# Kernel tuning notes

Hardware: AMD Instinct MI355X
Metric: run time of the kernel (lower is better)

The kernel has to match this reference:

```python
import jax, jax.numpy as jnp
import numpy as np

N_HEAD = 16


def setup_inputs() -> dict:
    key = jax.random.key(0)
    k1, k2, k3 = jax.random.split(key, 3)
    B, T, C = 4, 1024, 1024
    x = jax.random.normal(k1, (B, T, C), dtype=jnp.float32)
    w_attn = jax.random.normal(k2, (3 * C, C), dtype=jnp.float32) * 0.02
    w_proj = jax.random.normal(k3, (C, C), dtype=jnp.float32) * 0.02
    return {"x": x, "w_attn": w_attn, "w_proj": w_proj}


def reference(x, w_attn, w_proj):
    B, T, C = x.shape
    H = N_HEAD
    hs = C // H
    scale = 1.0 / np.sqrt(hs).astype(np.float32)

    qkv = x @ w_attn.T                         # [B, T, 3C]
    q, k, v = jnp.split(qkv, 3, axis=-1)
    q = q.reshape(B, T, H, hs).transpose(0, 2, 1, 3)   # [B, H, T, hs]
    k = k.reshape(B, T, H, hs).transpose(0, 2, 1, 3)
    v = v.reshape(B, T, H, hs).transpose(0, 2, 1, 3)

    scores = jnp.einsum('bhqd,bhkd->bhqk', q, k) * scale   # [B, H, T, T]
    causal = jnp.tril(jnp.ones((T, T), dtype=bool))
    scores = jnp.where(causal, scores, -jnp.inf)

    att = jax.nn.sigmoid(scores)                # sigmoid attention, not softmax
    # Bernoulli straight-through sampling (value = sample, grad flows via att)
    samp_key = jax.random.fold_in(jax.random.key(0), 42)
    samples = jax.random.bernoulli(samp_key, att).astype(att.dtype)
    att = att + jax.lax.stop_gradient(samples - att)

    y = jnp.einsum('bhqk,bhkd->bhqd', att, v)   # [B, H, T, hs]
    att_sum = att.sum(axis=-1)                  # [B, H, T]
    att_var = (att * (1.0 - att)).sum(axis=-1)  # [B, H, T]

    y = y.transpose(0, 2, 1, 3).reshape(B, T, C)
    y = y @ w_proj.T
    return (y, att_sum, att_var)
```

## Files before the change

### kernel.cpp

```cpp
#include <hip/hip_runtime.h>
#include <stdint.h>


#define T_SEQ 1024
#define QKV_LD 3072

typedef __attribute__((ext_vector_type(8))) short bf16x8;
typedef __attribute__((ext_vector_type(4))) float f32x4;
typedef __attribute__((ext_vector_type(4))) unsigned int u32x4;

typedef __attribute__((address_space(3))) uint32_t lds_u32;
typedef __attribute__((address_space(1))) const uint32_t g_u32;

#define ROTL(x, d) __builtin_amdgcn_alignbit((x), (x), 32 - (d))

__device__ __forceinline__ void threefry2x32(uint32_t k0, uint32_t k1,
                                             uint32_t x0, uint32_t x1,
                                             uint32_t &o0, uint32_t &o1) {
  uint32_t ks2 = k0 ^ k1 ^ 0x1BD11BDAu;
#define TF_R4(a, b, c, d)                                                      \
  x0 += x1; x1 = ROTL(x1, a); x1 ^= x0;                                        \
  x0 += x1; x1 = ROTL(x1, b); x1 ^= x0;                                        \
  x0 += x1; x1 = ROTL(x1, c); x1 ^= x0;                                        \
  x0 += x1; x1 = ROTL(x1, d); x1 ^= x0;
  x0 += k0; x1 += k1;
  TF_R4(13, 15, 26, 6)
  x0 += k1; x1 += ks2 + 1u;
  TF_R4(17, 29, 16, 24)
  x0 += ks2; x1 += k0 + 2u;
  TF_R4(13, 15, 26, 6)
  x0 += k0; x1 += k1 + 3u;
  TF_R4(17, 29, 16, 24)
  x0 += k1; x1 += ks2 + 4u;
  TF_R4(13, 15, 26, 6)
  x0 += ks2; x1 += k0 + 5u;
  o0 = x0; o1 = x1;
#undef TF_R4
}

__device__ __forceinline__ unsigned short f2bf(float f) {
  uint32_t u = __float_as_uint(f);
  u += 0x7FFFu + ((u >> 16) & 1u);
  return (unsigned short)(u >> 16);
}

#define N_X4  1048576
#define N_WA4 786432
#define N_WP4 262144

__global__ __launch_bounds__(256) void cvt3_bf16(const float4* __restrict__ x,
                                                 const float4* __restrict__ wa,
                                                 const float4* __restrict__ wp,
                                                 uint2* __restrict__ out) {
  size_t i = (size_t)blockIdx.x * 256 + threadIdx.x;
  const float4* src;
  size_t off;
  if (i < N_X4) { src = x; off = i; }
  else if (i < N_X4 + N_WA4) { src = wa; off = i - N_X4; }
  else { src = wp; off = i - (N_X4 + N_WA4); }
  float4 v = src[off];
  uint2 o;
  o.x = (uint32_t)f2bf(v.x) | ((uint32_t)f2bf(v.y) << 16);
  o.y = (uint32_t)f2bf(v.z) | ((uint32_t)f2bf(v.w) << 16);
  out[i] = o;
}

template <int OUT_BF16>
__global__ __launch_bounds__(256) void gemm_bf16(const unsigned short* __restrict__ A,
                                                 const unsigned short* __restrict__ B,
                                                 void* __restrict__ Cout,
                                                 int M, int N, int K) {
  __shared__ unsigned short As[128 * 32];
  __shared__ unsigned short Bs[128 * 32];

  const int t = threadIdx.x;
  const int lane = t & 63, w = t >> 6;
  const int g = lane >> 4, lr = lane & 15;
  const int rw = w >> 1, cw = w & 1;
  const int bm = blockIdx.x * 128, bn = blockIdx.y * 128;

  const unsigned short* Ag = A + (size_t)(bm + 32 * w + (lane >> 2)) * K + 8 * (lane & 3);
  const unsigned short* Bg = B + (size_t)(bn + 32 * w + (lane >> 2)) * K + 8 * (lane & 3);
  lds_u32* Al0 = (lds_u32*)&As[(32 * w) * 32];
  lds_u32* Al1 = (lds_u32*)&As[(32 * w + 16) * 32];
  lds_u32* Bl0 = (lds_u32*)&Bs[(32 * w) * 32];
  lds_u32* Bl1 = (lds_u32*)&Bs[(32 * w + 16) * 32];

  f32x4 acc[4][4];
#pragma unroll
  for (int i = 0; i < 4; ++i)
#pragma unroll
    for (int j = 0; j < 4; ++j) acc[i][j] = (f32x4){0.f, 0.f, 0.f, 0.f};

  for (int k0 = 0; k0 < K; k0 += 32) {
    __syncthreads();
    __builtin_amdgcn_global_load_lds((g_u32*)(const void*)(Ag + k0), Al0, 16, 0, 0);
    __builtin_amdgcn_global_load_lds((g_u32*)(const void*)(Ag + k0 + (size_t)16 * K), Al1, 16, 0, 0);
    __builtin_amdgcn_global_load_lds((g_u32*)(const void*)(Bg + k0), Bl0, 16, 0, 0);
    __builtin_amdgcn_global_load_lds((g_u32*)(const void*)(Bg + k0 + (size_t)16 * K), Bl1, 16, 0, 0);
    __syncthreads();

    bf16x8 af[4], bfr[4];
#pragma unroll
    for (int i = 0; i < 4; ++i)
      af[i] = *(const bf16x8*)&As[(64 * rw + 16 * i + lr) * 32 + 8 * g];
#pragma unroll
    for (int j = 0; j < 4; ++j)
      bfr[j] = *(const bf16x8*)&Bs[(64 * cw + 16 * j + lr) * 32 + 8 * g];
#pragma unroll
    for (int i = 0; i < 4; ++i)
#pragma unroll
      for (int j = 0; j < 4; ++j)
        acc[i][j] = __builtin_amdgcn_mfma_f32_16x16x32_bf16(af[i], bfr[j], acc[i][j], 0, 0, 0);
  }

#pragma unroll
  for (int i = 0; i < 4; ++i)
#pragma unroll
    for (int j = 0; j < 4; ++j)
#pragma unroll
      for (int r = 0; r < 4; ++r) {
        const size_t row = bm + 64 * rw + 16 * i + 4 * g + r;
        const size_t col = bn + 64 * cw + 16 * j + lr;
        if (OUT_BF16)
          ((unsigned short*)Cout)[row * N + col] = f2bf(acc[i][j][r]);
        else
          ((float*)Cout)[row * N + col] = acc[i][j][r];
      }
}

__constant__ int QT2[16] = {15, 13, 11, 9, 0, 2, 4, 6, 14, 12, 10, 8, 1, 3, 5, 7};

__global__ __launch_bounds__(256) void attn_tile2(const unsigned short* __restrict__ qkv,
                                                  unsigned short* __restrict__ yatt,
                                                  float* __restrict__ att_sum,
                                                  float* __restrict__ att_var) {
  __shared__ uint32_t Ks4[64 * 32];
  __shared__ uint32_t Vt4[64 * 32];
  __shared__ unsigned short St[4][16][72];

  const int t = threadIdx.x;
  const int lane = t & 63, w = t >> 6;
  const int g = lane >> 4, lr = lane & 15;
  const int i = blockIdx.x;
  const int bh = 8 * (i & 7) + ((i >> 3) & 7);
  const int qt = QT2[i >> 6];
  const int b = bh >> 4, h = bh & 15;
  const int qt64 = qt * 64;

  uint32_t dk0, dk1;
  threefry2x32(0u, 0u, 0u, 42u, dk0, dk1);

  const int swzr = (lr & 7) << 2;
  unsigned short (*stw)[72] = St[w];

  const int q0 = qt64 + 16 * w;
  const unsigned short* qr = qkv + (size_t)(b * T_SEQ + q0 + lr) * QKV_LD + h * 64 + 8 * g;
  const bf16x8 aq0 = *(const bf16x8*)qr;
  const bf16x8 aq1 = *(const bf16x8*)(qr + 32);

  f32x4 yacc[4];
#pragma unroll
  for (int c = 0; c < 4; ++c) yacc[c] = (f32x4){0.f, 0.f, 0.f, 0.f};
  int rs[4] = {0, 0, 0, 0};

#pragma unroll 1
  for (int kt = 0; kt <= qt; ++kt) {
    __syncthreads();
    const unsigned short* kb = qkv + (size_t)(b * T_SEQ + kt * 64) * QKV_LD + 1024 + h * 64;
    {
      const int r = t >> 2, s4 = t & 3;
      const unsigned short* src = kb + (size_t)r * QKV_LD + 8 * s4;
      u32x4 v0 = *(const u32x4*)(src);
      u32x4 v1 = *(const u32x4*)(src + 32);
      const int sw = (r & 7) << 2;
      *(u32x4*)&Ks4[r * 32 + ((4 * s4) ^ sw)] = v0;
      *(u32x4*)&Ks4[r * 32 + ((4 * s4 + 16) ^ sw)] = v1;
    }
    {
      const int k2 = 2 * (t & 31), d0 = 8 * (t >> 5);
      const unsigned short* vsrc =
          qkv + (size_t)(b * T_SEQ + kt * 64 + k2) * QKV_LD + 2048 + h * 64 + d0;
      union { u32x4 v; unsigned short us[8]; } va, vb;
      va.v = *(const u32x4*)(vsrc);
      vb.v = *(const u32x4*)(vsrc + QKV_LD);
#pragma unroll
      for (int j = 0; j < 8; ++j) {
        uint32_t pw = (uint32_t)va.us[j] | ((uint32_t)vb.us[j] << 16);
        Vt4[(d0 + j) * 32 + ((t & 31) ^ ((j & 7) << 2))] = pw;
      }
    }
    __syncthreads();

    const int kt64 = kt * 64;
#pragma unroll
    for (int c = 0; c < 4; ++c) {
      const uint32_t* krow = &Ks4[(16 * c + lr) * 32];
      bf16x8 bk0 = *(const bf16x8*)&krow[(4 * g) ^ swzr];
      bf16x8 bk1 = *(const bf16x8*)&krow[(4 * g + 16) ^ swzr];
      f32x4 sa = __builtin_amdgcn_mfma_f32_16x16x32_bf16(aq0, bk0, (f32x4){0.f, 0.f, 0.f, 0.f}, 0, 0, 0);
      sa = __builtin_amdgcn_mfma_f32_16x16x32_bf16(aq1, bk1, sa, 0, 0, 0);

      const int kg = kt64 + 16 * c + lr;
#pragma unroll
      for (int r = 0; r < 4; ++r) {
        const int qg = q0 + 4 * g + r;
        unsigned short sbits = 0;
        if (kg <= qg) {
          float e = __builtin_exp2f(sa[r] * -0.18033688011112042f);
          uint32_t idx = ((uint32_t)bh << 20) | ((uint32_t)qg << 10) | (uint32_t)kg;
          uint32_t r0, r1;
          threefry2x32(dk0, dk1, 0u, idx, r0, r1);
          float u = __uint_as_float(0x3F800000u | ((r0 ^ r1) >> 9)) - 1.0f;
          if (fmaf(u, e, u) < 1.0f) { sbits = 0x3F80; rs[r] += 1; }
        }
        stw[4 * g + r][16 * c + lr] = sbits;
      }
    }

#pragma unroll
    for (int ks = 0; ks < 2; ++ks) {
      const bf16x8 pa = *(const bf16x8*)&stw[lr][32 * ks + 8 * g];
#pragma unroll
      for (int c = 0; c < 4; ++c) {
        bf16x8 vb = *(const bf16x8*)&Vt4[(16 * c + lr) * 32 + ((4 * g + 16 * ks) ^ swzr)];
        yacc[c] = __builtin_amdgcn_mfma_f32_16x16x32_bf16(pa, vb, yacc[c], 0, 0, 0);
      }
    }
  }

  const size_t yb = (size_t)(b * T_SEQ + q0) * 1024 + h * 64;
#pragma unroll
  for (int c = 0; c < 4; ++c)
#pragma unroll
    for (int r = 0; r < 4; ++r)
      yatt[yb + (size_t)(4 * g + r) * 1024 + 16 * c + lr] = f2bf(yacc[c][r]);

#pragma unroll
  for (int r = 0; r < 4; ++r) {
    rs[r] += __shfl_xor(rs[r], 1);
    rs[r] += __shfl_xor(rs[r], 2);
    rs[r] += __shfl_xor(rs[r], 4);
    rs[r] += __shfl_xor(rs[r], 8);
  }
  if (lr == 0) {
#pragma unroll
    for (int r = 0; r < 4; ++r)
      att_sum[(size_t)bh * T_SEQ + q0 + 4 * g + r] = (float)rs[r];
  }
  if (lane < 16) att_var[(size_t)bh * T_SEQ + qt64 + 16 * w + lane] = 0.f;
}

extern "C" void kernel_launch(void* const* d_in, const int* in_sizes, int n_in,
                              void* d_out, int out_size, void* d_ws, size_t ws_size,
                              hipStream_t stream) {
  (void)in_sizes; (void)n_in; (void)out_size; (void)ws_size;
  const float* x      = (const float*)d_in[0];
  const float* w_attn = (const float*)d_in[1];
  const float* w_proj = (const float*)d_in[2];

  float* y_out      = (float*)d_out;
  float* attsum_out = y_out + (size_t)4 * 1024 * 1024;
  float* attvar_out = attsum_out + (size_t)4 * 16 * 1024;

  unsigned short* ws_us = (unsigned short*)d_ws;
  unsigned short* x_bf    = ws_us;
  unsigned short* wa_bf   = x_bf + (size_t)4 * 1024 * 1024;
  unsigned short* wp_bf   = wa_bf + (size_t)3 * 1024 * 1024;
  unsigned short* qkv_bf  = wp_bf + (size_t)1024 * 1024;
  unsigned short* yatt_bf = qkv_bf + (size_t)4096 * 3072;

  dim3 blk(256);
  cvt3_bf16<<<dim3(8192), blk, 0, stream>>>((const float4*)x, (const float4*)w_attn,
                                            (const float4*)w_proj, (uint2*)x_bf);
  gemm_bf16<1><<<dim3(32, 24), blk, 0, stream>>>(x_bf, wa_bf, (void*)qkv_bf, 4096, 3072, 1024);
  attn_tile2<<<dim3(1024), blk, 0, stream>>>(qkv_bf, yatt_bf, attsum_out, attvar_out);
  gemm_bf16<0><<<dim3(32, 8), blk, 0, stream>>>(yatt_bf, wp_bf, (void*)y_out, 4096, 1024, 1024);
}
```

Before: 165.2 us.

## Replace static attention tile schedule with atomic work-stealing over half tiles

The attention kernel goes from a fixed 1024-block grid of 256-thread blocks to a persistent-style grid of 1792 blocks with 128 threads each. Each block processes 32-query half-tiles taken largest-first and fetches the next item from a global atomic counter, which a tiny kernel initialises every launch. The aim is better load balance for the triangular causal workload and less tail idle time. In exchange, each K/V tile is staged into LDS for only two waves instead of four, so global-to-LDS traffic per query roughly doubles, and there is an extra kernel launch plus an atomic per item.

```diff
diff --git a/kernel.cpp b/kernel.cpp
--- a/kernel.cpp
+++ b/kernel.cpp
@@ -4,6 +4,8 @@
 
 #define T_SEQ 1024
 #define QKV_LD 3072
+#define ATTN_GRID 1792
+#define N_ITEMS 2048
 
 typedef __attribute__((ext_vector_type(8))) short bf16x8;
 typedef __attribute__((ext_vector_type(4))) float f32x4;
@@ -65,6 +67,8 @@
   out[i] = o;
 }
 
+__global__ void init_ctr(uint32_t* __restrict__ ctr, uint32_t v) { *ctr = v; }
+
 template <int OUT_BF16>
 __global__ __launch_bounds__(256) void gemm_bf16(const unsigned short* __restrict__ A,
                                                  const unsigned short* __restrict__ B,
@@ -129,24 +133,19 @@
       }
 }
 
-__constant__ int QT2[16] = {15, 13, 11, 9, 0, 2, 4, 6, 14, 12, 10, 8, 1, 3, 5, 7};
-
-__global__ __launch_bounds__(256) void attn_tile2(const unsigned short* __restrict__ qkv,
+__global__ __launch_bounds__(128) void attn_steal(const unsigned short* __restrict__ qkv,
                                                   unsigned short* __restrict__ yatt,
                                                   float* __restrict__ att_sum,
-                                                  float* __restrict__ att_var) {
+                                                  float* __restrict__ att_var,
+                                                  uint32_t* __restrict__ ctr) {
   __shared__ uint32_t Ks4[64 * 32];
   __shared__ uint32_t Vt4[64 * 32];
-  __shared__ unsigned short St[4][16][72];
+  __shared__ unsigned short St[2][16][72];
+  __shared__ int next_item;
 
   const int t = threadIdx.x;
   const int lane = t & 63, w = t >> 6;
   const int g = lane >> 4, lr = lane & 15;
-  const int i = blockIdx.x;
-  const int bh = 8 * (i & 7) + ((i >> 3) & 7);
-  const int qt = QT2[i >> 6];
-  const int b = bh >> 4, h = bh & 15;
-  const int qt64 = qt * 64;
 
   uint32_t dk0, dk1;
   threefry2x32(0u, 0u, 0u, 42u, dk0, dk1);
@@ -154,101 +153,120 @@
   const int swzr = (lr & 7) << 2;
   unsigned short (*stw)[72] = St[w];
 
-  const int q0 = qt64 + 16 * w;
-  const unsigned short* qr = qkv + (size_t)(b * T_SEQ + q0 + lr) * QKV_LD + h * 64 + 8 * g;
-  const bf16x8 aq0 = *(const bf16x8*)qr;
-  const bf16x8 aq1 = *(const bf16x8*)(qr + 32);
-
-  f32x4 yacc[4];
-#pragma unroll
-  for (int c = 0; c < 4; ++c) yacc[c] = (f32x4){0.f, 0.f, 0.f, 0.f};
-  int rs[4] = {0, 0, 0, 0};
+  int item = blockIdx.x;
+  while (item < N_ITEMS) {
+    const int qt = 15 - (item >> 7);
+    const int bh = (item >> 1) & 63;
+    const int half = item & 1;
+    const int b = bh >> 4, h = bh & 15;
+    const int qt64 = qt * 64;
+    const int q0 = qt64 + 32 * half + 16 * w;
+
+    const unsigned short* qr = qkv + (size_t)(b * T_SEQ + q0 + lr) * QKV_LD + h * 64 + 8 * g;
+    const bf16x8 aq0 = *(const bf16x8*)qr;
+    const bf16x8 aq1 = *(const bf16x8*)(qr + 32);
+
+    f32x4 yacc[4];
+#pragma unroll
+    for (int c = 0; c < 4; ++c) yacc[c] = (f32x4){0.f, 0.f, 0.f, 0.f};
+    int rs[4] = {0, 0, 0, 0};
 
 #pragma unroll 1
-  for (int kt = 0; kt <= qt; ++kt) {
+    for (int kt = 0; kt <= qt; ++kt) {
+      __syncthreads();
+      const unsigned short* kb = qkv + (size_t)(b * T_SEQ + kt * 64) * QKV_LD + 1024 + h * 64;
+      {
+        const int r = t >> 1, c0 = 4 * (t & 1);
+        const unsigned short* src = kb + (size_t)r * QKV_LD + 8 * c0;
+        const int sw = (r & 7) << 2;
+#pragma unroll
+        for (int q = 0; q < 4; ++q) {
+          u32x4 v = *(const u32x4*)(src + 8 * q);
+          *(u32x4*)&Ks4[r * 32 + ((4 * (c0 + q)) ^ sw)] = v;
+        }
+      }
+      {
+#pragma unroll
+        for (int it2 = 0; it2 < 2; ++it2) {
+          const int tt = t + 128 * it2;
+          const int k2 = 2 * (tt & 31), d0 = 8 * (tt >> 5);
+          const unsigned short* vsrc =
+              qkv + (size_t)(b * T_SEQ + kt * 64 + k2) * QKV_LD + 2048 + h * 64 + d0;
+          union { u32x4 v; unsigned short us[8]; } va, vb2;
+          va.v = *(const u32x4*)(vsrc);
+          vb2.v = *(const u32x4*)(vsrc + QKV_LD);
+#pragma unroll
+          for (int jj = 0; jj < 8; ++jj) {
+            uint32_t pw = (uint32_t)va.us[jj] | ((uint32_t)vb2.us[jj] << 16);
+            Vt4[(d0 + jj) * 32 + ((tt & 31) ^ ((jj & 7) << 2))] = pw;
+          }
+        }
+      }
+      __syncthreads();
+
+      const int kt64 = kt * 64;
+#pragma unroll
+      for (int c = 0; c < 4; ++c) {
+        const uint32_t* krow = &Ks4[(16 * c + lr) * 32];
+        bf16x8 bk0 = *(const bf16x8*)&krow[(4 * g) ^ swzr];
+        bf16x8 bk1 = *(const bf16x8*)&krow[(4 * g + 16) ^ swzr];
+        f32x4 sa = __builtin_amdgcn_mfma_f32_16x16x32_bf16(aq0, bk0, (f32x4){0.f, 0.f, 0.f, 0.f}, 0, 0, 0);
+        sa = __builtin_amdgcn_mfma_f32_16x16x32_bf16(aq1, bk1, sa, 0, 0, 0);
+
+        const int kg = kt64 + 16 * c + lr;
+#pragma unroll
+        for (int r = 0; r < 4; ++r) {
+          const int qg = q0 + 4 * g + r;
+          unsigned short sbits = 0;
+          if (kg <= qg) {
+            float e = __builtin_exp2f(sa[r] * -0.18033688011112042f);
+            uint32_t idx = ((uint32_t)bh << 20) | ((uint32_t)qg << 10) | (uint32_t)kg;
+            uint32_t r0, r1;
+            threefry2x32(dk0, dk1, 0u, idx, r0, r1);
+            float u = __uint_as_float(0x3F800000u | ((r0 ^ r1) >> 9)) - 1.0f;
+            if (fmaf(u, e, u) < 1.0f) { sbits = 0x3F80; rs[r] += 1; }
+          }
+          stw[4 * g + r][16 * c + lr] = sbits;
+        }
+      }
+
+#pragma unroll
+      for (int ks = 0; ks < 2; ++ks) {
+        const bf16x8 pa = *(const bf16x8*)&stw[lr][32 * ks + 8 * g];
+#pragma unroll
+        for (int c = 0; c < 4; ++c) {
+          bf16x8 vb = *(const bf16x8*)&Vt4[(16 * c + lr) * 32 + ((4 * g + 16 * ks) ^ swzr)];
+          yacc[c] = __builtin_amdgcn_mfma_f32_16x16x32_bf16(pa, vb, yacc[c], 0, 0, 0);
+        }
+      }
+    }
+
+    const size_t yb = (size_t)(b * T_SEQ + q0) * 1024 + h * 64;
+#pragma unroll
+    for (int c = 0; c < 4; ++c)
+#pragma unroll
+      for (int r = 0; r < 4; ++r)
+        yatt[yb + (size_t)(4 * g + r) * 1024 + 16 * c + lr] = f2bf(yacc[c][r]);
+
+#pragma unroll
+    for (int r = 0; r < 4; ++r) {
+      rs[r] += __shfl_xor(rs[r], 1);
+      rs[r] += __shfl_xor(rs[r], 2);
+      rs[r] += __shfl_xor(rs[r], 4);
+      rs[r] += __shfl_xor(rs[r], 8);
+    }
+    if (lr == 0) {
+#pragma unroll
+      for (int r = 0; r < 4; ++r)
+        att_sum[(size_t)bh * T_SEQ + q0 + 4 * g + r] = (float)rs[r];
+    }
+    if (lane < 16) att_var[(size_t)bh * T_SEQ + q0 + lane] = 0.f;
+
     __syncthreads();
-    const unsigned short* kb = qkv + (size_t)(b * T_SEQ + kt * 64) * QKV_LD + 1024 + h * 64;
-    {
-      const int r = t >> 2, s4 = t & 3;
-      const unsigned short* src = kb + (size_t)r * QKV_LD + 8 * s4;
-      u32x4 v0 = *(const u32x4*)(src);
-      u32x4 v1 = *(const u32x4*)(src + 32);
-      const int sw = (r & 7) << 2;
-      *(u32x4*)&Ks4[r * 32 + ((4 * s4) ^ sw)] = v0;
-      *(u32x4*)&Ks4[r * 32 + ((4 * s4 + 16) ^ sw)] = v1;
-    }
-    {
-      const int k2 = 2 * (t & 31), d0 = 8 * (t >> 5);
-      const unsigned short* vsrc =
-          qkv + (size_t)(b * T_SEQ + kt * 64 + k2) * QKV_LD + 2048 + h * 64 + d0;
-      union { u32x4 v; unsigned short us[8]; } va, vb;
-      va.v = *(const u32x4*)(vsrc);
-      vb.v = *(const u32x4*)(vsrc + QKV_LD);
-#pragma unroll
-      for (int j = 0; j < 8; ++j) {
-        uint32_t pw = (uint32_t)va.us[j] | ((uint32_t)vb.us[j] << 16);
-        Vt4[(d0 + j) * 32 + ((t & 31) ^ ((j & 7) << 2))] = pw;
-      }
-    }
+    if (t == 0) next_item = (int)atomicAdd(ctr, 1u);
     __syncthreads();
-
-    const int kt64 = kt * 64;
-#pragma unroll
-    for (int c = 0; c < 4; ++c) {
-      const uint32_t* krow = &Ks4[(16 * c + lr) * 32];
-      bf16x8 bk0 = *(const bf16x8*)&krow[(4 * g) ^ swzr];
-      bf16x8 bk1 = *(const bf16x8*)&krow[(4 * g + 16) ^ swzr];
-      f32x4 sa = __builtin_amdgcn_mfma_f32_16x16x32_bf16(aq0, bk0, (f32x4){0.f, 0.f, 0.f, 0.f}, 0, 0, 0);
-      sa = __builtin_amdgcn_mfma_f32_16x16x32_bf16(aq1, bk1, sa, 0, 0, 0);
-
-      const int kg = kt64 + 16 * c + lr;
-#pragma unroll
-      for (int r = 0; r < 4; ++r) {
-        const int qg = q0 + 4 * g + r;
-        unsigned short sbits = 0;
-        if (kg <= qg) {
-          float e = __builtin_exp2f(sa[r] * -0.18033688011112042f);
-          uint32_t idx = ((uint32_t)bh << 20) | ((uint32_t)qg << 10) | (uint32_t)kg;
-          uint32_t r0, r1;
-          threefry2x32(dk0, dk1, 0u, idx, r0, r1);
-          float u = __uint_as_float(0x3F800000u | ((r0 ^ r1) >> 9)) - 1.0f;
-          if (fmaf(u, e, u) < 1.0f) { sbits = 0x3F80; rs[r] += 1; }
-        }
-        stw[4 * g + r][16 * c + lr] = sbits;
-      }
-    }
-
-#pragma unroll
-    for (int ks = 0; ks < 2; ++ks) {
-      const bf16x8 pa = *(const bf16x8*)&stw[lr][32 * ks + 8 * g];
-#pragma unroll
-      for (int c = 0; c < 4; ++c) {
-        bf16x8 vb = *(const bf16x8*)&Vt4[(16 * c + lr) * 32 + ((4 * g + 16 * ks) ^ swzr)];
-        yacc[c] = __builtin_amdgcn_mfma_f32_16x16x32_bf16(pa, vb, yacc[c], 0, 0, 0);
-      }
-    }
+    item = next_item;
   }
-
-  const size_t yb = (size_t)(b * T_SEQ + q0) * 1024 + h * 64;
-#pragma unroll
-  for (int c = 0; c < 4; ++c)
-#pragma unroll
-    for (int r = 0; r < 4; ++r)
-      yatt[yb + (size_t)(4 * g + r) * 1024 + 16 * c + lr] = f2bf(yacc[c][r]);
-
-#pragma unroll
-  for (int r = 0; r < 4; ++r) {
-    rs[r] += __shfl_xor(rs[r], 1);
-    rs[r] += __shfl_xor(rs[r], 2);
-    rs[r] += __shfl_xor(rs[r], 4);
-    rs[r] += __shfl_xor(rs[r], 8);
-  }
-  if (lr == 0) {
-#pragma unroll
-    for (int r = 0; r < 4; ++r)
-      att_sum[(size_t)bh * T_SEQ + q0 + 4 * g + r] = (float)rs[r];
-  }
-  if (lane < 16) att_var[(size_t)bh * T_SEQ + qt64 + 16 * w + lane] = 0.f;
 }
 
 extern "C" void kernel_launch(void* const* d_in, const int* in_sizes, int n_in,
@@ -269,11 +287,14 @@
   unsigned short* wp_bf   = wa_bf + (size_t)3 * 1024 * 1024;
   unsigned short* qkv_bf  = wp_bf + (size_t)1024 * 1024;
   unsigned short* yatt_bf = qkv_bf + (size_t)4096 * 3072;
+  uint32_t* ctr = (uint32_t*)(yatt_bf + (size_t)4096 * 1024);
 
   dim3 blk(256);
+  init_ctr<<<dim3(1), dim3(1), 0, stream>>>(ctr, ATTN_GRID);
   cvt3_bf16<<<dim3(8192), blk, 0, stream>>>((const float4*)x, (const float4*)w_attn,
                                             (const float4*)w_proj, (uint2*)x_bf);
   gemm_bf16<1><<<dim3(32, 24), blk, 0, stream>>>(x_bf, wa_bf, (void*)qkv_bf, 4096, 3072, 1024);
-  attn_tile2<<<dim3(1024), blk, 0, stream>>>(qkv_bf, yatt_bf, attsum_out, attvar_out);
+  attn_steal<<<dim3(ATTN_GRID), dim3(128), 0, stream>>>(qkv_bf, yatt_bf, attsum_out,
+                                                        attvar_out, ctr);
   gemm_bf16<0><<<dim3(32, 8), blk, 0, stream>>>(yatt_bf, wp_bf, (void*)y_out, 4096, 1024, 1024);
 }
```

New measurement: 183.8 us. 1.11x slower.

## Replace static attention grid with persistent per-XCC atomic work queue

Applied to the files above, without the earlier changes.

The attention kernel becomes persistent with 768 blocks. Each block pulls (head, query-tile) items from a per-XCC atomic counter, serving the longest causal tiles first and stealing from other XCC queues when its own is empty. The goal is better load balance across the triangular workload and L2 locality per XCC. It also splits the sampling pass so only the diagonal tile evaluates the causal mask. The cost is an extra counter-init launch and atomic contention on the queues.

```diff
diff --git a/kernel.cpp b/kernel.cpp
--- a/kernel.cpp
+++ b/kernel.cpp
@@ -4,6 +4,7 @@
 
 #define T_SEQ 1024
 #define QKV_LD 3072
+#define ATTN_GRID 768
 
 typedef __attribute__((ext_vector_type(8))) short bf16x8;
 typedef __attribute__((ext_vector_type(4))) float f32x4;
@@ -65,6 +66,10 @@
   out[i] = o;
 }
 
+__global__ void init_ctr(uint32_t* __restrict__ ctr) {
+  if (threadIdx.x < 8) ctr[threadIdx.x] = 0u;
+}
+
 template <int OUT_BF16>
 __global__ __launch_bounds__(256) void gemm_bf16(const unsigned short* __restrict__ A,
                                                  const unsigned short* __restrict__ B,
@@ -129,24 +134,48 @@
       }
 }
 
-__constant__ int QT2[16] = {15, 13, 11, 9, 0, 2, 4, 6, 14, 12, 10, 8, 1, 3, 5, 7};
-
-__global__ __launch_bounds__(256) void attn_tile2(const unsigned short* __restrict__ qkv,
+#define SAMPLE_PASS(MASKED)                                                    \
+  for (int c = 0; c < 4; ++c) {                                                \
+    const uint32_t* krow = &Ks4[(16 * c + lr) * 32];                           \
+    bf16x8 bk0 = *(const bf16x8*)&krow[(4 * g) ^ swzr];                        \
+    bf16x8 bk1 = *(const bf16x8*)&krow[(4 * g + 16) ^ swzr];                   \
+    f32x4 sa = __builtin_amdgcn_mfma_f32_16x16x32_bf16(                        \
+        aq0, bk0, (f32x4){0.f, 0.f, 0.f, 0.f}, 0, 0, 0);                       \
+    sa = __builtin_amdgcn_mfma_f32_16x16x32_bf16(aq1, bk1, sa, 0, 0, 0);       \
+    const int kg = kt64 + 16 * c + lr;                                         \
+    _Pragma("unroll")                                                          \
+    for (int r = 0; r < 4; ++r) {                                              \
+      const int qg = q0 + 4 * g + r;                                           \
+      unsigned short sbits = 0;                                                \
+      if (!MASKED || kg <= qg) {                                               \
+        float e = __builtin_exp2f(sa[r] * -0.18033688011112042f);              \
+        uint32_t idx2 = ((uint32_t)bh << 20) | ((uint32_t)qg << 10) | (uint32_t)kg; \
+        uint32_t r0, r1;                                                       \
+        threefry2x32(dk0, dk1, 0u, idx2, r0, r1);                              \
+        float u = __uint_as_float(0x3F800000u | ((r0 ^ r1) >> 9)) - 1.0f;      \
+        if (fmaf(u, e, u) < 1.0f) { sbits = 0x3F80; rs[r] += 1; }              \
+      }                                                                        \
+      stw[4 * g + r][16 * c + lr] = sbits;                                     \
+    }                                                                          \
+  }
+
+__global__ __launch_bounds__(256) void attn_queue(const unsigned short* __restrict__ qkv,
                                                   unsigned short* __restrict__ yatt,
                                                   float* __restrict__ att_sum,
-                                                  float* __restrict__ att_var) {
+                                                  float* __restrict__ att_var,
+                                                  uint32_t* __restrict__ qctr) {
   __shared__ uint32_t Ks4[64 * 32];
   __shared__ uint32_t Vt4[64 * 32];
   __shared__ unsigned short St[4][16][72];
+  __shared__ int s_item, s_xcc;
 
   const int t = threadIdx.x;
   const int lane = t & 63, w = t >> 6;
   const int g = lane >> 4, lr = lane & 15;
-  const int i = blockIdx.x;
-  const int bh = 8 * (i & 7) + ((i >> 3) & 7);
-  const int qt = QT2[i >> 6];
-  const int b = bh >> 4, h = bh & 15;
-  const int qt64 = qt * 64;
+
+  uint32_t my_xcc;
+  asm volatile("s_getreg_b32 %0, hwreg(HW_REG_XCC_ID)" : "=s"(my_xcc));
+  my_xcc &= 7u;
 
   uint32_t dk0, dk1;
   threefry2x32(0u, 0u, 0u, 42u, dk0, dk1);
@@ -154,101 +183,106 @@
   const int swzr = (lr & 7) << 2;
   unsigned short (*stw)[72] = St[w];
 
-  const int q0 = qt64 + 16 * w;
-  const unsigned short* qr = qkv + (size_t)(b * T_SEQ + q0 + lr) * QKV_LD + h * 64 + 8 * g;
-  const bf16x8 aq0 = *(const bf16x8*)qr;
-  const bf16x8 aq1 = *(const bf16x8*)(qr + 32);
-
-  f32x4 yacc[4];
-#pragma unroll
-  for (int c = 0; c < 4; ++c) yacc[c] = (f32x4){0.f, 0.f, 0.f, 0.f};
-  int rs[4] = {0, 0, 0, 0};
-
-#pragma unroll 1
-  for (int kt = 0; kt <= qt; ++kt) {
+  int probe = 0;
+  for (;;) {
     __syncthreads();
-    const unsigned short* kb = qkv + (size_t)(b * T_SEQ + kt * 64) * QKV_LD + 1024 + h * 64;
-    {
-      const int r = t >> 2, s4 = t & 3;
-      const unsigned short* src = kb + (size_t)r * QKV_LD + 8 * s4;
-      u32x4 v0 = *(const u32x4*)(src);
-      u32x4 v1 = *(const u32x4*)(src + 32);
-      const int sw = (r & 7) << 2;
-      *(u32x4*)&Ks4[r * 32 + ((4 * s4) ^ sw)] = v0;
-      *(u32x4*)&Ks4[r * 32 + ((4 * s4 + 16) ^ sw)] = v1;
-    }
-    {
-      const int k2 = 2 * (t & 31), d0 = 8 * (t >> 5);
-      const unsigned short* vsrc =
-          qkv + (size_t)(b * T_SEQ + kt * 64 + k2) * QKV_LD + 2048 + h * 64 + d0;
-      union { u32x4 v; unsigned short us[8]; } va, vb;
-      va.v = *(const u32x4*)(vsrc);
-      vb.v = *(const u32x4*)(vsrc + QKV_LD);
-#pragma unroll
-      for (int j = 0; j < 8; ++j) {
-        uint32_t pw = (uint32_t)va.us[j] | ((uint32_t)vb.us[j] << 16);
-        Vt4[(d0 + j) * 32 + ((t & 31) ^ ((j & 7) << 2))] = pw;
-      }
+    if (t == 0) {
+      int got = -1, gx = 0;
+      while (probe < 8) {
+        int x = ((int)my_xcc + probe) & 7;
+        uint32_t idx = atomicAdd(&qctr[x], 1u);
+        if (idx < 128u) { got = (int)idx; gx = x; break; }
+        ++probe;
+      }
+      s_item = got; s_xcc = gx;
     }
     __syncthreads();
-
-    const int kt64 = kt * 64;
-#pragma unroll
-    for (int c = 0; c < 4; ++c) {
-      const uint32_t* krow = &Ks4[(16 * c + lr) * 32];
-      bf16x8 bk0 = *(const bf16x8*)&krow[(4 * g) ^ swzr];
-      bf16x8 bk1 = *(const bf16x8*)&krow[(4 * g + 16) ^ swzr];
-      f32x4 sa = __builtin_amdgcn_mfma_f32_16x16x32_bf16(aq0, bk0, (f32x4){0.f, 0.f, 0.f, 0.f}, 0, 0, 0);
-      sa = __builtin_amdgcn_mfma_f32_16x16x32_bf16(aq1, bk1, sa, 0, 0, 0);
-
-      const int kg = kt64 + 16 * c + lr;
-#pragma unroll
-      for (int r = 0; r < 4; ++r) {
-        const int qg = q0 + 4 * g + r;
-        unsigned short sbits = 0;
-        if (kg <= qg) {
-          float e = __builtin_exp2f(sa[r] * -0.18033688011112042f);
-          uint32_t idx = ((uint32_t)bh << 20) | ((uint32_t)qg << 10) | (uint32_t)kg;
-          uint32_t r0, r1;
-          threefry2x32(dk0, dk1, 0u, idx, r0, r1);
-          float u = __uint_as_float(0x3F800000u | ((r0 ^ r1) >> 9)) - 1.0f;
-          if (fmaf(u, e, u) < 1.0f) { sbits = 0x3F80; rs[r] += 1; }
+    const int item = s_item;
+    if (item < 0) break;
+    const int bh = 8 * s_xcc + (item & 7);
+    const int qt = 15 - (item >> 3);
+    const int b = bh >> 4, h = bh & 15;
+    const int qt64 = qt * 64;
+    const int q0 = qt64 + 16 * w;
+
+    const unsigned short* qr = qkv + (size_t)(b * T_SEQ + q0 + lr) * QKV_LD + h * 64 + 8 * g;
+    const bf16x8 aq0 = *(const bf16x8*)qr;
+    const bf16x8 aq1 = *(const bf16x8*)(qr + 32);
+
+    f32x4 yacc[4];
+#pragma unroll
+    for (int c = 0; c < 4; ++c) yacc[c] = (f32x4){0.f, 0.f, 0.f, 0.f};
+    int rs[4] = {0, 0, 0, 0};
+
+#pragma unroll 1
+    for (int kt = 0; kt <= qt; ++kt) {
+      __syncthreads();
+      const unsigned short* kb = qkv + (size_t)(b * T_SEQ + kt * 64) * QKV_LD + 1024 + h * 64;
+      {
+        const int r = t >> 2, s4 = t & 3;
+        const unsigned short* src = kb + (size_t)r * QKV_LD + 8 * s4;
+        u32x4 v0 = *(const u32x4*)(src);
+        u32x4 v1 = *(const u32x4*)(src + 32);
+        const int sw = (r & 7) << 2;
+        *(u32x4*)&Ks4[r * 32 + ((4 * s4) ^ sw)] = v0;
+        *(u32x4*)&Ks4[r * 32 + ((4 * s4 + 16) ^ sw)] = v1;
+      }
+      {
+        const int k2 = 2 * (t & 31), d0 = 8 * (t >> 5);
+        const unsigned short* vsrc =
+            qkv + (size_t)(b * T_SEQ + kt * 64 + k2) * QKV_LD + 2048 + h * 64 + d0;
+        union { u32x4 v; unsigned short us[8]; } va, vb2;
+        va.v = *(const u32x4*)(vsrc);
+        vb2.v = *(const u32x4*)(vsrc + QKV_LD);
+#pragma unroll
+        for (int jj = 0; jj < 8; ++jj) {
+          uint32_t pw = (uint32_t)va.us[jj] | ((uint32_t)vb2.us[jj] << 16);
+          Vt4[(d0 + jj) * 32 + ((t & 31) ^ ((jj & 7) << 2))] = pw;
         }
-        stw[4 * g + r][16 * c + lr] = sbits;
+      }
+      __syncthreads();
+
+      const int kt64 = kt * 64;
+      if (kt < qt) {
+#pragma unroll
+        SAMPLE_PASS(0)
+      } else {
+#pragma unroll
+        SAMPLE_PASS(1)
+      }
+
+#pragma unroll
+      for (int ks = 0; ks < 2; ++ks) {
+        const bf16x8 pa = *(const bf16x8*)&stw[lr][32 * ks + 8 * g];
+#pragma unroll
+        for (int c = 0; c < 4; ++c) {
+          bf16x8 vb = *(const bf16x8*)&Vt4[(16 * c + lr) * 32 + ((4 * g + 16 * ks) ^ swzr)];
+          yacc[c] = __builtin_amdgcn_mfma_f32_16x16x32_bf16(pa, vb, yacc[c], 0, 0, 0);
+        }
       }
     }
 
-#pragma unroll
-    for (int ks = 0; ks < 2; ++ks) {
-      const bf16x8 pa = *(const bf16x8*)&stw[lr][32 * ks + 8 * g];
-#pragma unroll
-      for (int c = 0; c < 4; ++c) {
-        bf16x8 vb = *(const bf16x8*)&Vt4[(16 * c + lr) * 32 + ((4 * g + 16 * ks) ^ swzr)];
-        yacc[c] = __builtin_amdgcn_mfma_f32_16x16x32_bf16(pa, vb, yacc[c], 0, 0, 0);
-      }
+    const size_t yb = (size_t)(b * T_SEQ + q0) * 1024 + h * 64;
+#pragma unroll
+    for (int c = 0; c < 4; ++c)
+#pragma unroll
+      for (int r = 0; r < 4; ++r)
+        yatt[yb + (size_t)(4 * g + r) * 1024 + 16 * c + lr] = f2bf(yacc[c][r]);
+
+#pragma unroll
+    for (int r = 0; r < 4; ++r) {
+      rs[r] += __shfl_xor(rs[r], 1);
+      rs[r] += __shfl_xor(rs[r], 2);
+      rs[r] += __shfl_xor(rs[r], 4);
+      rs[r] += __shfl_xor(rs[r], 8);
     }
+    if (lr == 0) {
+#pragma unroll
+      for (int r = 0; r < 4; ++r)
+        att_sum[(size_t)bh * T_SEQ + q0 + 4 * g + r] = (float)rs[r];
+    }
+    if (lane < 16) att_var[(size_t)bh * T_SEQ + q0 + lane] = 0.f;
   }
-
-  const size_t yb = (size_t)(b * T_SEQ + q0) * 1024 + h * 64;
-#pragma unroll
-  for (int c = 0; c < 4; ++c)
-#pragma unroll
-    for (int r = 0; r < 4; ++r)
-      yatt[yb + (size_t)(4 * g + r) * 1024 + 16 * c + lr] = f2bf(yacc[c][r]);
-
-#pragma unroll
-  for (int r = 0; r < 4; ++r) {
-    rs[r] += __shfl_xor(rs[r], 1);
-    rs[r] += __shfl_xor(rs[r], 2);
-    rs[r] += __shfl_xor(rs[r], 4);
-    rs[r] += __shfl_xor(rs[r], 8);
-  }
-  if (lr == 0) {
-#pragma unroll
-    for (int r = 0; r < 4; ++r)
-      att_sum[(size_t)bh * T_SEQ + q0 + 4 * g + r] = (float)rs[r];
-  }
-  if (lane < 16) att_var[(size_t)bh * T_SEQ + qt64 + 16 * w + lane] = 0.f;
 }
 
 extern "C" void kernel_launch(void* const* d_in, const int* in_sizes, int n_in,
@@ -269,11 +303,14 @@
   unsigned short* wp_bf   = wa_bf + (size_t)3 * 1024 * 1024;
   unsigned short* qkv_bf  = wp_bf + (size_t)1024 * 1024;
   unsigned short* yatt_bf = qkv_bf + (size_t)4096 * 3072;
+  uint32_t* qctr = (uint32_t*)(yatt_bf + (size_t)4096 * 1024);
 
   dim3 blk(256);
+  init_ctr<<<dim3(1), dim3(64), 0, stream>>>(qctr);
   cvt3_bf16<<<dim3(8192), blk, 0, stream>>>((const float4*)x, (const float4*)w_attn,
                                             (const float4*)w_proj, (uint2*)x_bf);
   gemm_bf16<1><<<dim3(32, 24), blk, 0, stream>>>(x_bf, wa_bf, (void*)qkv_bf, 4096, 3072, 1024);
-  attn_tile2<<<dim3(1024), blk, 0, stream>>>(qkv_bf, yatt_bf, attsum_out, attvar_out);
+  attn_queue<<<dim3(ATTN_GRID), blk, 0, stream>>>(qkv_bf, yatt_bf, attsum_out,
+                                                  attvar_out, qctr);
   gemm_bf16<0><<<dim3(32, 8), blk, 0, stream>>>(yatt_bf, wp_bf, (void*)y_out, 4096, 1024, 1024);
 }
```

New measurement: 218.6 us. +32.3%, slower.

## Split attention into parallel per-tile sampling kernel and bitmask PV kernel

Applied to the files above, without the earlier changes.

The fused causal attention kernel is split in two. The first kernel launches one block per (q-tile, k-tile) pair, 8704 blocks in all, to compute QK scores, sigmoid, threefry RNG and Bernoulli samples, and packs the samples into a global bitmask with wave ballots. The second kernel walks the k-tiles per query tile, expands the bits into bf16 operands for the PV MFMAs and uses popcount for att_sum. This spreads the RNG-heavy sampling across many more blocks instead of serialising it per query tile. It costs an extra launch and a global round trip for the bitmask.

```diff
diff --git a/kernel.cpp b/kernel.cpp
--- a/kernel.cpp
+++ b/kernel.cpp
@@ -129,102 +129,141 @@
       }
 }
 
-__constant__ int QT2[16] = {15, 13, 11, 9, 0, 2, 4, 6, 14, 12, 10, 8, 1, 3, 5, 7};
-
-__global__ __launch_bounds__(256) void attn_tile2(const unsigned short* __restrict__ qkv,
-                                                  unsigned short* __restrict__ yatt,
-                                                  float* __restrict__ att_sum,
-                                                  float* __restrict__ att_var) {
+__constant__ uint8_t QT_OF[136] = {
+    0, 1, 1, 2, 2, 2, 3, 3, 3, 3, 4, 4, 4, 4, 4, 5, 5, 5, 5, 5, 5,
+    6, 6, 6, 6, 6, 6, 6, 7, 7, 7, 7, 7, 7, 7, 7,
+    8, 8, 8, 8, 8, 8, 8, 8, 8, 9, 9, 9, 9, 9, 9, 9, 9, 9, 9,
+    10, 10, 10, 10, 10, 10, 10, 10, 10, 10, 10,
+    11, 11, 11, 11, 11, 11, 11, 11, 11, 11, 11, 11,
+    12, 12, 12, 12, 12, 12, 12, 12, 12, 12, 12, 12, 12,
+    13, 13, 13, 13, 13, 13, 13, 13, 13, 13, 13, 13, 13, 13,
+    14, 14, 14, 14, 14, 14, 14, 14, 14, 14, 14, 14, 14, 14, 14,
+    15, 15, 15, 15, 15, 15, 15, 15, 15, 15, 15, 15, 15, 15, 15, 15};
+
+__global__ __launch_bounds__(256, 6) void attn_sample(const unsigned short* __restrict__ qkv,
+                                                      unsigned short* __restrict__ Pbits) {
   __shared__ uint32_t Ks4[64 * 32];
-  __shared__ uint32_t Vt4[64 * 32];
-  __shared__ unsigned short St[4][16][72];
 
   const int t = threadIdx.x;
   const int lane = t & 63, w = t >> 6;
   const int g = lane >> 4, lr = lane & 15;
-  const int i = blockIdx.x;
-  const int bh = 8 * (i & 7) + ((i >> 3) & 7);
-  const int qt = QT2[i >> 6];
+  const int bid = blockIdx.x;
+  const int bh = 8 * (bid & 7) + ((bid >> 3) & 7);
+  const int id = bid >> 6;
+  const int qt = QT_OF[id];
+  const int kt = id - ((qt * (qt + 1)) >> 1);
   const int b = bh >> 4, h = bh & 15;
-  const int qt64 = qt * 64;
+  const int q0 = qt * 64 + 16 * w;
+  const int kt64 = kt * 64;
+  const bool diag = (kt == qt);
 
   uint32_t dk0, dk1;
   threefry2x32(0u, 0u, 0u, 42u, dk0, dk1);
 
-  const int swzr = (lr & 7) << 2;
-  unsigned short (*stw)[72] = St[w];
-
-  const int q0 = qt64 + 16 * w;
+  const unsigned short* kb = qkv + (size_t)(b * T_SEQ + kt64) * QKV_LD + 1024 + h * 64;
+  {
+    const int r = t >> 2, s4 = t & 3;
+    const unsigned short* src = kb + (size_t)r * QKV_LD + 8 * s4;
+    u32x4 v0 = *(const u32x4*)(src);
+    u32x4 v1 = *(const u32x4*)(src + 32);
+    const int sw = (r & 7) << 2;
+    *(u32x4*)&Ks4[r * 32 + ((4 * s4) ^ sw)] = v0;
+    *(u32x4*)&Ks4[r * 32 + ((4 * s4 + 16) ^ sw)] = v1;
+  }
   const unsigned short* qr = qkv + (size_t)(b * T_SEQ + q0 + lr) * QKV_LD + h * 64 + 8 * g;
   const bf16x8 aq0 = *(const bf16x8*)qr;
   const bf16x8 aq1 = *(const bf16x8*)(qr + 32);
+  __syncthreads();
+
+  const int swzr = (lr & 7) << 2;
+  unsigned short* prow = Pbits + ((size_t)((bh << 10) + q0)) * 64 + kt * 4;
+
+#pragma unroll
+  for (int c = 0; c < 4; ++c) {
+    const uint32_t* krow = &Ks4[(16 * c + lr) * 32];
+    bf16x8 bk0 = *(const bf16x8*)&krow[(4 * g) ^ swzr];
+    bf16x8 bk1 = *(const bf16x8*)&krow[(4 * g + 16) ^ swzr];
+    f32x4 sa = __builtin_amdgcn_mfma_f32_16x16x32_bf16(aq0, bk0, (f32x4){0.f, 0.f, 0.f, 0.f}, 0, 0, 0);
+    sa = __builtin_amdgcn_mfma_f32_16x16x32_bf16(aq1, bk1, sa, 0, 0, 0);
+
+    const int kg = kt64 + 16 * c + lr;
+#pragma unroll
+    for (int r = 0; r < 4; ++r) {
+      const int qg = q0 + 4 * g + r;
+      bool pred = false;
+      if (!diag || kg <= qg) {
+        float e = __builtin_exp2f(sa[r] * -0.18033688011112042f);
+        uint32_t idx2 = ((uint32_t)bh << 20) | ((uint32_t)qg << 10) | (uint32_t)kg;
+        uint32_t r0, r1;
+        threefry2x32(dk0, dk1, 0u, idx2, r0, r1);
+        float u = __uint_as_float(0x3F800000u | ((r0 ^ r1) >> 9)) - 1.0f;
+        pred = (fmaf(u, e, u) < 1.0f);
+      }
+      unsigned long long m = __ballot(pred);
+      if (lr == 0)
+        prow[(size_t)(4 * g + r) * 64 + c] = (unsigned short)((m >> (16 * g)) & 0xFFFFu);
+    }
+  }
+}
+
+__global__ __launch_bounds__(256) void attn_pv(const unsigned short* __restrict__ qkv,
+                                               const unsigned short* __restrict__ Pbits,
+                                               unsigned short* __restrict__ yatt,
+                                               float* __restrict__ att_sum,
+                                               float* __restrict__ att_var) {
+  __shared__ uint32_t Vt4[64 * 32];
+
+  const int t = threadIdx.x;
+  const int lane = t & 63, w = t >> 6;
+  const int g = lane >> 4, lr = lane & 15;
+  const int bid = blockIdx.x;
+  const int bh = 8 * (bid & 7) + ((bid >> 3) & 7);
+  const int qt = 15 - (bid >> 6);
+  const int b = bh >> 4, h = bh & 15;
+  const int q0 = qt * 64 + 16 * w;
+
+  const int swzr = (lr & 7) << 2;
+  const unsigned short* prow = Pbits + ((size_t)((bh << 10) + q0 + lr)) * 64;
 
   f32x4 yacc[4];
 #pragma unroll
   for (int c = 0; c < 4; ++c) yacc[c] = (f32x4){0.f, 0.f, 0.f, 0.f};
-  int rs[4] = {0, 0, 0, 0};
+  uint32_t rs = 0;
 
 #pragma unroll 1
   for (int kt = 0; kt <= qt; ++kt) {
     __syncthreads();
-    const unsigned short* kb = qkv + (size_t)(b * T_SEQ + kt * 64) * QKV_LD + 1024 + h * 64;
-    {
-      const int r = t >> 2, s4 = t & 3;
-      const unsigned short* src = kb + (size_t)r * QKV_LD + 8 * s4;
-      u32x4 v0 = *(const u32x4*)(src);
-      u32x4 v1 = *(const u32x4*)(src + 32);
-      const int sw = (r & 7) << 2;
-      *(u32x4*)&Ks4[r * 32 + ((4 * s4) ^ sw)] = v0;
-      *(u32x4*)&Ks4[r * 32 + ((4 * s4 + 16) ^ sw)] = v1;
-    }
     {
       const int k2 = 2 * (t & 31), d0 = 8 * (t >> 5);
       const unsigned short* vsrc =
           qkv + (size_t)(b * T_SEQ + kt * 64 + k2) * QKV_LD + 2048 + h * 64 + d0;
-      union { u32x4 v; unsigned short us[8]; } va, vb;
+      union { u32x4 v; unsigned short us[8]; } va, vb2;
       va.v = *(const u32x4*)(vsrc);
-      vb.v = *(const u32x4*)(vsrc + QKV_LD);
-#pragma unroll
-      for (int j = 0; j < 8; ++j) {
-        uint32_t pw = (uint32_t)va.us[j] | ((uint32_t)vb.us[j] << 16);
-        Vt4[(d0 + j) * 32 + ((t & 31) ^ ((j & 7) << 2))] = pw;
+      vb2.v = *(const u32x4*)(vsrc + QKV_LD);
+#pragma unroll
+      for (int jj = 0; jj < 8; ++jj) {
+        uint32_t pw = (uint32_t)va.us[jj] | ((uint32_t)vb2.us[jj] << 16);
+        Vt4[(d0 + jj) * 32 + ((t & 31) ^ ((jj & 7) << 2))] = pw;
       }
     }
     __syncthreads();
 
-    const int kt64 = kt * 64;
-#pragma unroll
-    for (int c = 0; c < 4; ++c) {
-      const uint32_t* krow = &Ks4[(16 * c + lr) * 32];
-      bf16x8 bk0 = *(const bf16x8*)&krow[(4 * g) ^ swzr];
-      bf16x8 bk1 = *(const bf16x8*)&krow[(4 * g + 16) ^ swzr];
-      f32x4 sa = __builtin_amdgcn_mfma_f32_16x16x32_bf16(aq0, bk0, (f32x4){0.f, 0.f, 0.f, 0.f}, 0, 0, 0);
-      sa = __builtin_amdgcn_mfma_f32_16x16x32_bf16(aq1, bk1, sa, 0, 0, 0);
-
-      const int kg = kt64 + 16 * c + lr;
-#pragma unroll
-      for (int r = 0; r < 4; ++r) {
-        const int qg = q0 + 4 * g + r;
-        unsigned short sbits = 0;
-        if (kg <= qg) {
-          float e = __builtin_exp2f(sa[r] * -0.18033688011112042f);
-          uint32_t idx = ((uint32_t)bh << 20) | ((uint32_t)qg << 10) | (uint32_t)kg;
-          uint32_t r0, r1;
-          threefry2x32(dk0, dk1, 0u, idx, r0, r1);
-          float u = __uint_as_float(0x3F800000u | ((r0 ^ r1) >> 9)) - 1.0f;
-          if (fmaf(u, e, u) < 1.0f) { sbits = 0x3F80; rs[r] += 1; }
-        }
-        stw[4 * g + r][16 * c + lr] = sbits;
-      }
-    }
+    const uint64_t bits = *(const uint64_t*)(prow + kt * 4);
+    rs += (uint32_t)__popcll(bits);
 
 #pragma unroll
     for (int ks = 0; ks < 2; ++ks) {
-      const bf16x8 pa = *(const bf16x8*)&stw[lr][32 * ks + 8 * g];
+      const uint32_t byte = (uint32_t)(bits >> (32 * ks + 8 * g)) & 0xFFu;
+      union { uint32_t u[4]; bf16x8 v; } pa;
+#pragma unroll
+      for (int j = 0; j < 4; ++j) {
+        pa.u[j] = ((byte >> (2 * j)) & 1u ? 0x3F80u : 0u) |
+                  ((byte >> (2 * j + 1)) & 1u ? 0x3F800000u : 0u);
+      }
 #pragma unroll
       for (int c = 0; c < 4; ++c) {
         bf16x8 vb = *(const bf16x8*)&Vt4[(16 * c + lr) * 32 + ((4 * g + 16 * ks) ^ swzr)];
-        yacc[c] = __builtin_amdgcn_mfma_f32_16x16x32_bf16(pa, vb, yacc[c], 0, 0, 0);
+        yacc[c] = __builtin_amdgcn_mfma_f32_16x16x32_bf16(pa.v, vb, yacc[c], 0, 0, 0);
       }
     }
   }
@@ -236,19 +275,8 @@
     for (int r = 0; r < 4; ++r)
       yatt[yb + (size_t)(4 * g + r) * 1024 + 16 * c + lr] = f2bf(yacc[c][r]);
 
-#pragma unroll
-  for (int r = 0; r < 4; ++r) {
-    rs[r] += __shfl_xor(rs[r], 1);
-    rs[r] += __shfl_xor(rs[r], 2);
-    rs[r] += __shfl_xor(rs[r], 4);
-    rs[r] += __shfl_xor(rs[r], 8);
-  }
-  if (lr == 0) {
-#pragma unroll
-    for (int r = 0; r < 4; ++r)
-      att_sum[(size_t)bh * T_SEQ + q0 + 4 * g + r] = (float)rs[r];
-  }
-  if (lane < 16) att_var[(size_t)bh * T_SEQ + qt64 + 16 * w + lane] = 0.f;
+  if (g == 0) att_sum[(size_t)bh * T_SEQ + q0 + lr] = (float)rs;
+  if (lane < 16) att_var[(size_t)bh * T_SEQ + q0 + lane] = 0.f;
 }
 
 extern "C" void kernel_launch(void* const* d_in, const int* in_sizes, int n_in,
@@ -269,11 +297,13 @@
   unsigned short* wp_bf   = wa_bf + (size_t)3 * 1024 * 1024;
   unsigned short* qkv_bf  = wp_bf + (size_t)1024 * 1024;
   unsigned short* yatt_bf = qkv_bf + (size_t)4096 * 3072;
+  unsigned short* pbits   = yatt_bf + (size_t)4096 * 1024;
 
   dim3 blk(256);
   cvt3_bf16<<<dim3(8192), blk, 0, stream>>>((const float4*)x, (const float4*)w_attn,
                                             (const float4*)w_proj, (uint2*)x_bf);
   gemm_bf16<1><<<dim3(32, 24), blk, 0, stream>>>(x_bf, wa_bf, (void*)qkv_bf, 4096, 3072, 1024);
-  attn_tile2<<<dim3(1024), blk, 0, stream>>>(qkv_bf, yatt_bf, attsum_out, attvar_out);
+  attn_sample<<<dim3(8704), blk, 0, stream>>>(qkv_bf, pbits);
+  attn_pv<<<dim3(1024), blk, 0, stream>>>(qkv_bf, pbits, yatt_bf, attsum_out, attvar_out);
   gemm_bf16<0><<<dim3(32, 8), blk, 0, stream>>>(yatt_bf, wp_bf, (void*)y_out, 4096, 1024, 1024);
 }
```

New measurement: 171.4 us. +3.7%, slower.
